# Kernel tuning notes

Hardware: AMD Instinct MI355X
Metric: run time of the kernel (lower is better)

The kernel has to match this reference:

```python
import jax, jax.numpy as jnp
import numpy as np

D_MODEL = 4096
N_Q_HEADS = 32
N_KV_HEADS = 8
HEAD_DIM = D_MODEL // N_Q_HEADS  # 128
N_REP = N_Q_HEADS // N_KV_HEADS  # 4
BATCH = 2
SEQ = 2048
ROPE_THETA = 10000.0


def setup_inputs() -> dict:
    key = jax.random.key(0)
    ks = jax.random.split(key, 5)
    scale = 0.02
    x = jax.random.normal(ks[0], (BATCH, SEQ, D_MODEL), dtype=jnp.float32)
    w_q = jax.random.normal(ks[1], (D_MODEL, N_Q_HEADS * HEAD_DIM), dtype=jnp.float32) * scale
    w_k = jax.random.normal(ks[2], (D_MODEL, N_KV_HEADS * HEAD_DIM), dtype=jnp.float32) * scale
    w_v = jax.random.normal(ks[3], (D_MODEL, N_KV_HEADS * HEAD_DIM), dtype=jnp.float32) * scale
    w_o = jax.random.normal(ks[4], (N_Q_HEADS * HEAD_DIM, D_MODEL), dtype=jnp.float32) * scale
    # precompute_theta_pos_freqs: freqs_cis = exp(1j * outer(t, inv_freq))
    inv_freq = 1.0 / (ROPE_THETA ** (jnp.arange(0, HEAD_DIM, 2)[: HEAD_DIM // 2] / HEAD_DIM))
    t = jnp.arange(SEQ, dtype=jnp.float32)
    freqs = jnp.outer(t, inv_freq)  # [S, HEAD_DIM//2]
    freqs_cos = jnp.cos(freqs).astype(jnp.float32)
    freqs_sin = jnp.sin(freqs).astype(jnp.float32)
    # additive causal mask [1,1,S,S]
    causal = jnp.tril(jnp.ones((SEQ, SEQ), dtype=bool))
    mask = jnp.where(causal, 0.0, -1e9).astype(jnp.float32)[None, None]
    return {"x": x, "w_q": w_q, "w_k": w_k, "w_v": w_v, "w_o": w_o,
            "freqs_cos": freqs_cos, "freqs_sin": freqs_sin, "mask": mask}


def _apply_rope(t, cos, sin):
    # t: [B,S,H,D]; cos/sin: [S,D//2]. Complex multiply in real arithmetic:
    # (a + bi) * (c + di) = (ac - bd) + (ad + bc)i
    B, S, H, D = t.shape
    tr = t.reshape(B, S, H, D // 2, 2)
    a, b = tr[..., 0], tr[..., 1]
    c = cos[None, :, None, :]
    s = sin[None, :, None, :]
    out = jnp.stack([a * c - b * s, a * s + b * c], axis=-1)
    return out.reshape(B, S, H, D)


def reference(x, w_q, w_k, w_v, w_o, freqs_cos, freqs_sin, mask):
    B, S, _ = x.shape
    xq = (x @ w_q).reshape(B, S, N_Q_HEADS, HEAD_DIM)
    xk = (x @ w_k).reshape(B, S, N_KV_HEADS, HEAD_DIM)
    xv = (x @ w_v).reshape(B, S, N_KV_HEADS, HEAD_DIM)
    xq = _apply_rope(xq, freqs_cos, freqs_sin)
    xk = _apply_rope(xk, freqs_cos, freqs_sin)
    # repeat_kv (tile+reshape == repeat along head axis)
    keys = jnp.repeat(xk, N_REP, axis=2)    # [B,S,Hq,D]
    values = jnp.repeat(xv, N_REP, axis=2)  # [B,S,Hq,D]
    xq = xq.transpose(0, 2, 1, 3)           # [B,Hq,S,D]
    keys = keys.transpose(0, 2, 1, 3)
    values = values.transpose(0, 2, 1, 3)
    scores = jnp.einsum("bhqd,bhkd->bhqk", xq, keys) / jnp.sqrt(
        jnp.asarray(HEAD_DIM, dtype=xq.dtype))
    scores = scores + mask
    probs = jax.nn.softmax(scores, axis=-1).astype(xq.dtype)
    out = jnp.einsum("bhqk,bhkd->bhqd", probs, values)
    out = out.transpose(0, 2, 1, 3).reshape(B, S, N_Q_HEADS * HEAD_DIM)
    return out @ w_o


if __name__ == "__main__":
    inp = setup_inputs()
    y = reference(**inp)
    print(y.shape, y.dtype)
```

## Files before the change

kernel.cpp:

```cpp
#include <hip/hip_runtime.h>
#include <stdint.h>
#include <stddef.h>


typedef __bf16 bf16x8 __attribute__((ext_vector_type(8)));
typedef float floatx4 __attribute__((ext_vector_type(4)));
typedef unsigned short ushort8v __attribute__((ext_vector_type(8)));
typedef unsigned short ushort4v __attribute__((ext_vector_type(4)));
typedef unsigned short ushort2v __attribute__((ext_vector_type(2)));

#define DEV static __device__ __forceinline__

DEV unsigned short f2bf(float f) {
  union { float f; unsigned u; } v; v.f = f;
  unsigned r = v.u + 0x7fffu + ((v.u >> 16) & 1u);
  return (unsigned short)(r >> 16);
}
DEV float bf2f(unsigned short b) {
  union { unsigned u; float f; } v; v.u = ((unsigned)b) << 16;
  return v.f;
}

DEV void gload_lds16(const void* g, void* lds) {
  __builtin_amdgcn_global_load_lds(
      (__attribute__((address_space(1))) void*)(g),
      (__attribute__((address_space(3))) void*)(lds), 16, 0, 0);
}

__global__ __launch_bounds__(256) void cvt_fp32_bf16(
    const float* __restrict__ in, unsigned short* __restrict__ out, int n4) {
  int i = blockIdx.x * 256 + threadIdx.x;
  if (i >= n4) return;
  float4 v = ((const float4*)in)[i];
  ushort4v w;
  w.x = f2bf(v.x); w.y = f2bf(v.y); w.z = f2bf(v.z); w.w = f2bf(v.w);
  *(ushort4v*)(out + (size_t)i * 4) = w;
}

__global__ __launch_bounds__(256) void transpose_cvt(
    const float* __restrict__ in, unsigned short* __restrict__ out, int K, int N) {
  __shared__ float tile[32][33];
  int k0 = blockIdx.x * 32, n0 = blockIdx.y * 32;
  int tx = threadIdx.x & 31, ty = threadIdx.x >> 5;
  for (int i = 0; i < 32; i += 8)
    tile[ty + i][tx] = in[(size_t)(k0 + ty + i) * N + n0 + tx];
  __syncthreads();
  for (int i = 0; i < 32; i += 8)
    out[(size_t)(n0 + ty + i) * K + k0 + tx] = f2bf(tile[tx][ty + i]);
}

template <int STORE_F32>
__global__ __launch_bounds__(256, 2) void gemm_bt(
    const unsigned short* __restrict__ A, const unsigned short* __restrict__ Bt,
    void* __restrict__ Cp, int M, int N, int K) {
  __shared__ __align__(16) unsigned short a_lds[4096];
  __shared__ __align__(16) unsigned short b_lds[4096];
  const int tid = threadIdx.x;
  const int wave = tid >> 6, lane = tid & 63;
  const int quad = lane >> 4, l16 = lane & 15;
  const int m0 = blockIdx.x * 128, n0 = blockIdx.y * 128;
  const int wm = (wave >> 1) * 64, wn = (wave & 1) * 64;

  const int srow = (lane >> 2);
  const int skq = (lane & 3) ^ ((lane >> 2) & 3);

  floatx4 acc[4][4] = {};

  for (int k0 = 0; k0 < K; k0 += 32) {
    __syncthreads();
    for (int s = 0; s < 2; ++s) {
      int t = wave * 2 + s;
      int row = t * 16 + srow;
      gload_lds16(A + (size_t)(m0 + row) * K + k0 + skq * 8, a_lds + t * 512);
      gload_lds16(Bt + (size_t)(n0 + row) * K + k0 + skq * 8, b_lds + t * 512);
    }
    __syncthreads();
    bf16x8 af[4], bfr[4];
    const int pos = (quad ^ (l16 & 3)) * 8;
    for (int i = 0; i < 4; ++i)
      af[i] = *(const bf16x8*)(a_lds + (wm + i * 16 + l16) * 32 + pos);
    for (int j = 0; j < 4; ++j)
      bfr[j] = *(const bf16x8*)(b_lds + (wn + j * 16 + l16) * 32 + pos);
    for (int i = 0; i < 4; ++i)
      for (int j = 0; j < 4; ++j)
        acc[i][j] =
            __builtin_amdgcn_mfma_f32_16x16x32_bf16(af[i], bfr[j], acc[i][j], 0, 0, 0);
  }

  for (int i = 0; i < 4; ++i)
    for (int j = 0; j < 4; ++j)
      for (int r = 0; r < 4; ++r) {
        int row = m0 + wm + i * 16 + quad * 4 + r;
        int col = n0 + wn + j * 16 + l16;
        float v = acc[i][j][r];
        if (STORE_F32)
          ((float*)Cp)[(size_t)row * N + col] = v;
        else
          ((unsigned short*)Cp)[(size_t)row * N + col] = f2bf(v);
      }
}

__global__ __launch_bounds__(256) void rope_q(
    const unsigned short* __restrict__ qkv, const float* __restrict__ fc,
    const float* __restrict__ fs, unsigned short* __restrict__ Qd) {
  int gid = blockIdx.x * 256 + threadIdx.x;
  int i = gid & 63;
  int h = (gid >> 6) & 31;
  int s = (gid >> 11) & 2047;
  int b = gid >> 22;
  int row = b * 2048 + s;
  ushort2v p = *(const ushort2v*)(qkv + (size_t)row * 6144 + h * 128 + 2 * i);
  float a = bf2f(p.x), bb = bf2f(p.y);
  float c = fc[s * 64 + i], sn = fs[s * 64 + i];
  ushort2v w;
  w.x = f2bf(a * c - bb * sn);
  w.y = f2bf(a * sn + bb * c);
  *(ushort2v*)(Qd + ((((size_t)b * 32 + h) * 2048 + s) * 128 + 2 * i)) = w;
}

__global__ __launch_bounds__(256) void rope_k(
    const unsigned short* __restrict__ qkv, const float* __restrict__ fc,
    const float* __restrict__ fs, unsigned short* __restrict__ Kd) {
  int gid = blockIdx.x * 256 + threadIdx.x;
  int i = gid & 63;
  int kvh = (gid >> 6) & 7;
  int s = (gid >> 9) & 2047;
  int b = gid >> 20;
  int row = b * 2048 + s;
  ushort2v p = *(const ushort2v*)(qkv + (size_t)row * 6144 + 4096 + kvh * 128 + 2 * i);
  float a = bf2f(p.x), bb = bf2f(p.y);
  float c = fc[s * 64 + i], sn = fs[s * 64 + i];
  ushort2v w;
  w.x = f2bf(a * c - bb * sn);
  w.y = f2bf(a * sn + bb * c);
  *(ushort2v*)(Kd + ((((size_t)b * 8 + kvh) * 2048 + s) * 128 + 2 * i)) = w;
}

__global__ __launch_bounds__(256) void vtrans(
    const unsigned short* __restrict__ qkv, unsigned short* __restrict__ Vt) {
  __shared__ unsigned short tile[32][33];
  int bk = blockIdx.z;
  int b = bk >> 3, kvh = bk & 7;
  int s0 = blockIdx.x * 32, d0 = blockIdx.y * 32;
  int tx = threadIdx.x & 31, ty = threadIdx.x >> 5;
  for (int i = 0; i < 32; i += 8)
    tile[ty + i][tx] =
        qkv[(size_t)(b * 2048 + s0 + ty + i) * 6144 + 5120 + kvh * 128 + d0 + tx];
  __syncthreads();
  for (int i = 0; i < 32; i += 8)
    Vt[((size_t)bk * 128 + d0 + ty + i) * 2048 + s0 + tx] = tile[tx][ty + i];
}

__global__ __launch_bounds__(512, 4) void attn_kernel(
    const unsigned short* __restrict__ Q,
    const unsigned short* __restrict__ Kd,
    const unsigned short* __restrict__ Vt,
    unsigned short* __restrict__ O) {
  __shared__ __align__(16) unsigned short k_lds[64][136];
  __shared__ __align__(16) unsigned short v_lds[128][72];
  __shared__ __align__(16) unsigned short p_lds[8][16][72];

  const int tid = threadIdx.x;
  const int wave = tid >> 6, lane = tid & 63;
  const int quad = lane >> 4, l16 = lane & 15;
  const int pr = blockIdx.x;
  const int h = blockIdx.y;
  const int b = blockIdx.z;
  const int kvh = h >> 2;
  const float scale = 0.08838834764831845f;

  const unsigned short* kbase = Kd + ((size_t)b * 8 + kvh) * 2048 * 128;
  const unsigned short* vbase = Vt + ((size_t)b * 8 + kvh) * 128 * 2048;

  const int kk = tid >> 4, kd = tid & 15;
  const int vd = tid >> 3, vs = tid & 7;

  for (int pass = 0; pass < 2; ++pass) {
    const int qt = pass == 0 ? pr : 15 - pr;
    const int q0 = qt * 128;

    const unsigned short* qrow =
        Q + (((size_t)b * 32 + h) * 2048 + q0 + wave * 16 + l16) * 128;
    bf16x8 qf[4];
    for (int t = 0; t < 4; ++t)
      qf[t] = *(const bf16x8*)(qrow + t * 32 + quad * 8);

    float m_i[4], l_i[4];
    for (int r = 0; r < 4; ++r) { m_i[r] = -3.0e38f; l_i[r] = 0.f; }
    floatx4 o_acc[8] = {};

    ushort8v krg[2], vrg[2];
    krg[0] = *(const ushort8v*)(kbase + (size_t)kk * 128 + kd * 8);
    krg[1] = *(const ushort8v*)(kbase + (size_t)(kk + 32) * 128 + kd * 8);
    vrg[0] = *(const ushort8v*)(vbase + (size_t)vd * 2048 + vs * 8);
    vrg[1] = *(const ushort8v*)(vbase + (size_t)(vd + 64) * 2048 + vs * 8);

    const int kb_last = q0 + 64;
    for (int kb = 0; kb <= kb_last; kb += 64) {
      __syncthreads();
      *(ushort8v*)&k_lds[kk][kd * 8] = krg[0];
      *(ushort8v*)&k_lds[kk + 32][kd * 8] = krg[1];
      *(ushort8v*)&v_lds[vd][vs * 8] = vrg[0];
      *(ushort8v*)&v_lds[vd + 64][vs * 8] = vrg[1];
      __syncthreads();
      if (kb < kb_last) {
        int nkb = kb + 64;
        krg[0] = *(const ushort8v*)(kbase + (size_t)(nkb + kk) * 128 + kd * 8);
        krg[1] = *(const ushort8v*)(kbase + (size_t)(nkb + kk + 32) * 128 + kd * 8);
        vrg[0] = *(const ushort8v*)(vbase + (size_t)vd * 2048 + nkb + vs * 8);
        vrg[1] = *(const ushort8v*)(vbase + (size_t)(vd + 64) * 2048 + nkb + vs * 8);
      }
      if (kb > q0 + wave * 16 + 15) continue;

      float sv[4][4];
      for (int kt = 0; kt < 4; ++kt) {
        floatx4 a = {0.f, 0.f, 0.f, 0.f};
        for (int t = 0; t < 4; ++t) {
          bf16x8 kf = *(const bf16x8*)&k_lds[kt * 16 + l16][t * 32 + quad * 8];
          a = __builtin_amdgcn_mfma_f32_16x16x32_bf16(qf[t], kf, a, 0, 0, 0);
        }
        for (int r = 0; r < 4; ++r) sv[kt][r] = a[r] * scale;
      }
      if (kb + 63 > q0 + wave * 16) {
        for (int kt = 0; kt < 4; ++kt) {
          int kcol = kb + kt * 16 + l16;
          for (int r = 0; r < 4; ++r) {
            int qg = q0 + wave * 16 + quad * 4 + r;
            if (kcol > qg) sv[kt][r] -= 1.0e9f;
          }
        }
      }
      float mx[4];
      for (int r = 0; r < 4; ++r) {
        float m = fmaxf(fmaxf(sv[0][r], sv[1][r]), fmaxf(sv[2][r], sv[3][r]));
        for (int off = 1; off < 16; off <<= 1)
          m = fmaxf(m, __shfl_xor(m, off));
        mx[r] = m;
      }
      bool grow = false;
      for (int r = 0; r < 4; ++r) grow |= (mx[r] > m_i[r] + 8.f);
      if (__any(grow)) {
        for (int r = 0; r < 4; ++r) {
          float mnew = fmaxf(m_i[r], mx[r]);
          float alpha = __expf(m_i[r] - mnew);
          m_i[r] = mnew;
          l_i[r] *= alpha;
          for (int nb = 0; nb < 8; ++nb) o_acc[nb][r] *= alpha;
        }
      }
      for (int r = 0; r < 4; ++r) {
        float sum = 0.f;
        for (int kt = 0; kt < 4; ++kt) {
          float p = __expf(sv[kt][r] - m_i[r]);
          sv[kt][r] = p;
          sum += p;
        }
        for (int off = 1; off < 16; off <<= 1)
          sum += __shfl_xor(sum, off);
        l_i[r] += sum;
      }
      for (int kt = 0; kt < 4; ++kt)
        for (int r = 0; r < 4; ++r)
          p_lds[wave][quad * 4 + r][kt * 16 + l16] = f2bf(sv[kt][r]);
      for (int tk = 0; tk < 2; ++tk) {
        bf16x8 pa = *(const bf16x8*)&p_lds[wave][l16][tk * 32 + quad * 8];
        for (int nb = 0; nb < 8; ++nb) {
          bf16x8 vb = *(const bf16x8*)&v_lds[nb * 16 + l16][tk * 32 + quad * 8];
          o_acc[nb] = __builtin_amdgcn_mfma_f32_16x16x32_bf16(pa, vb, o_acc[nb], 0, 0, 0);
        }
      }
    }

    for (int nb = 0; nb < 8; ++nb)
      for (int r = 0; r < 4; ++r) {
        int row = b * 2048 + q0 + wave * 16 + quad * 4 + r;
        int col = h * 128 + nb * 16 + l16;
        O[(size_t)row * 4096 + col] = f2bf(o_acc[nb][r] / l_i[r]);
      }
  }
}

extern "C" void kernel_launch(void* const* d_in, const int* in_sizes, int n_in,
                              void* d_out, int out_size, void* d_ws, size_t ws_size,
                              hipStream_t stream) {
  const float* x   = (const float*)d_in[0];
  const float* w_q = (const float*)d_in[1];
  const float* w_k = (const float*)d_in[2];
  const float* w_v = (const float*)d_in[3];
  const float* w_o = (const float*)d_in[4];
  const float* fc  = (const float*)d_in[5];
  const float* fs  = (const float*)d_in[6];
  (void)in_sizes; (void)n_in; (void)out_size; (void)ws_size;

  char* ws = (char*)d_ws;
  unsigned short* xb  = (unsigned short*)(ws);
  unsigned short* wT  = (unsigned short*)(ws + 33554432ull);
  unsigned short* qkv = (unsigned short*)(ws + 83886080ull);
  unsigned short* Kd  = (unsigned short*)(ws + 134217728ull);
  unsigned short* Vt  = (unsigned short*)(ws + 142606336ull);
  unsigned short* Qd  = xb;
  unsigned short* woT = wT;
  unsigned short* Ob  = qkv;

  cvt_fp32_bf16<<<16384, 256, 0, stream>>>(x, xb, 4194304);
  transpose_cvt<<<dim3(128, 128), 256, 0, stream>>>(w_q, wT, 4096, 4096);
  transpose_cvt<<<dim3(128, 32), 256, 0, stream>>>(w_k, wT + (size_t)4096 * 4096, 4096, 1024);
  transpose_cvt<<<dim3(128, 32), 256, 0, stream>>>(w_v, wT + (size_t)5120 * 4096, 4096, 1024);
  gemm_bt<0><<<dim3(32, 48), 256, 0, stream>>>(xb, wT, qkv, 4096, 6144, 4096);
  transpose_cvt<<<dim3(128, 128), 256, 0, stream>>>(w_o, woT, 4096, 4096);
  rope_q<<<32768, 256, 0, stream>>>(qkv, fc, fs, Qd);
  rope_k<<<8192, 256, 0, stream>>>(qkv, fc, fs, Kd);
  vtrans<<<dim3(64, 4, 16), 256, 0, stream>>>(qkv, Vt);
  attn_kernel<<<dim3(8, 32, 2), 512, 0, stream>>>(Qd, Kd, Vt, Ob);
  gemm_bt<1><<<dim3(32, 32), 256, 0, stream>>>(Ob, woT, d_out, 4096, 4096, 4096);
}
```

Measured before the change: 817.1 us.

## Replace GEMM with 256x256 tile, 8-wave, double-buffered ping-pong pipelined kernel

Replaces the 128x128 single-buffered GEMM with a 256x256-tile, 512-thread kernel. It uses K=64 double-buffered LDS with XOR swizzle, interleaves global-to-LDS staging with MFMA phases under barriers and s_setprio, and adds block-index swizzling for L2 locality. The aim is to raise arithmetic intensity and hide memory latency in the QKV and output projections. In exchange it uses 128KB of LDS and many more accumulator registers, and depends on hand-tuned vmcnt counts, so occupancy and correctness are sensitive.

New measurement: 794.3 us. 1.03x faster.

```diff
diff --git a/kernel.cpp b/kernel.cpp
--- a/kernel.cpp
+++ b/kernel.cpp
@@ -49,50 +49,132 @@
     out[(size_t)(n0 + ty + i) * K + k0 + tx] = f2bf(tile[tx][ty + i]);
 }
 
+#define LD8(LDS, D, ROW, Q)                                                  \
+  (*(const bf16x8*)((const char*)(LDS) + (D) * 32768 + (ROW) * 128 +         \
+                    (((Q) ^ ((ROW) & 7)) << 4)))
+
+#define STAGE(PANEL, LDS, KT, H)                                             \
+  {                                                                          \
+    _Pragma("unroll") for (int j_ = 0; j_ < 2; ++j_) {                       \
+      int t_ = wave * 2 + j_;                                                \
+      int row_ = (H) * 128 + t_ * 8 + srow;                                  \
+      gload_lds16(PANEL + (size_t)row_ * K + (size_t)(KT) * 64 + qsrc * 8,   \
+                  (char*)(LDS) + ((KT) & 1) * 32768 + (H) * 16384 +          \
+                      t_ * 1024);                                            \
+    }                                                                        \
+  }
+
+#define READ_A(D, MH)                                                        \
+  _Pragma("unroll") for (int mf_ = 0; mf_ < 4; ++mf_)                        \
+      _Pragma("unroll") for (int kk_ = 0; kk_ < 2; ++kk_)                    \
+          aR[mf_][kk_] =                                                     \
+      LD8(a_lds, D, wm + ((MH) * 4 + mf_) * 16 + l16, kk_ * 4 + quad);
+
+#define READ_B(D, NH, BREG)                                                  \
+  _Pragma("unroll") for (int nf_ = 0; nf_ < 2; ++nf_)                        \
+      _Pragma("unroll") for (int kk_ = 0; kk_ < 2; ++kk_)                    \
+          BREG[nf_][kk_] =                                                   \
+      LD8(b_lds, D, wn + ((NH) * 2 + nf_) * 16 + l16, kk_ * 4 + quad);
+
+#define MFMA_Q(MH, NH, BREG)                                                 \
+  _Pragma("unroll") for (int mf_ = 0; mf_ < 4; ++mf_)                        \
+      _Pragma("unroll") for (int nf_ = 0; nf_ < 2; ++nf_)                    \
+          _Pragma("unroll") for (int kk_ = 0; kk_ < 2; ++kk_)                \
+              acc[(MH) * 4 + mf_][(NH) * 2 + nf_] =                          \
+      __builtin_amdgcn_mfma_f32_16x16x32_bf16(                               \
+          aR[mf_][kk_], BREG[nf_][kk_],                                      \
+          acc[(MH) * 4 + mf_][(NH) * 2 + nf_], 0, 0, 0);
+
+#define PH_SYNC_BEGIN                                                        \
+  __builtin_amdgcn_s_barrier();                                              \
+  asm volatile("s_waitcnt lgkmcnt(0)" ::: "memory");                         \
+  __builtin_amdgcn_s_setprio(1);
+
+#define PH_SYNC_END                                                          \
+  __builtin_amdgcn_s_setprio(0);                                             \
+  __builtin_amdgcn_s_barrier();
+
 template <int STORE_F32>
-__global__ __launch_bounds__(256, 2) void gemm_bt(
+__global__ __launch_bounds__(512, 2) void gemm_bt8(
     const unsigned short* __restrict__ A, const unsigned short* __restrict__ Bt,
     void* __restrict__ Cp, int M, int N, int K) {
-  __shared__ __align__(16) unsigned short a_lds[4096];
-  __shared__ __align__(16) unsigned short b_lds[4096];
+  __shared__ __align__(16) unsigned short a_lds[32768];
+  __shared__ __align__(16) unsigned short b_lds[32768];
+
   const int tid = threadIdx.x;
   const int wave = tid >> 6, lane = tid & 63;
   const int quad = lane >> 4, l16 = lane & 15;
-  const int m0 = blockIdx.x * 128, n0 = blockIdx.y * 128;
-  const int wm = (wave >> 1) * 64, wn = (wave & 1) * 64;
-
-  const int srow = (lane >> 2);
-  const int skq = (lane & 3) ^ ((lane >> 2) & 3);
-
-  floatx4 acc[4][4] = {};
-
-  for (int k0 = 0; k0 < K; k0 += 32) {
-    __syncthreads();
-    for (int s = 0; s < 2; ++s) {
-      int t = wave * 2 + s;
-      int row = t * 16 + srow;
-      gload_lds16(A + (size_t)(m0 + row) * K + k0 + skq * 8, a_lds + t * 512);
-      gload_lds16(Bt + (size_t)(n0 + row) * K + k0 + skq * 8, b_lds + t * 512);
+  const int wm = (wave >> 2) * 128, wn = (wave & 3) * 64;
+
+  const int gx = gridDim.x, gy = gridDim.y;
+  int lid = blockIdx.y * gx + blockIdx.x;
+  int cpx = (gx * gy) >> 3;
+  int swz = (lid & 7) * cpx + (lid >> 3);
+  const int m0 = (swz / gy) * 256, n0 = (swz % gy) * 256;
+
+  const int qsrc = (lane & 7) ^ (lane >> 3);
+  const int srow = lane >> 3;
+  const unsigned short* Ab = A + (size_t)m0 * K;
+  const unsigned short* Bb = Bt + (size_t)n0 * K;
+
+  floatx4 acc[8][4] = {};
+  bf16x8 aR[4][2], bLo[2][2], bHi[2][2];
+
+  const int nt = K >> 6;
+  const int iters = nt >> 1;
+
+  STAGE(Ab, a_lds, 0, 0); STAGE(Ab, a_lds, 0, 1);
+  STAGE(Bb, b_lds, 0, 0); STAGE(Bb, b_lds, 0, 1);
+  STAGE(Bb, b_lds, 1, 0); STAGE(Bb, b_lds, 1, 1);
+  asm volatile("s_waitcnt vmcnt(0)" ::: "memory");
+  __builtin_amdgcn_s_barrier();
+
+  for (int i = 0; i < iters; ++i) {
+    const int t0 = 2 * i;
+    const bool has2 = (t0 + 2 < nt);
+    READ_A(0, 0); READ_B(0, 0, bLo);
+    STAGE(Ab, a_lds, t0 + 1, 0);
+    PH_SYNC_BEGIN; MFMA_Q(0, 0, bLo); PH_SYNC_END;
+    READ_B(0, 1, bHi);
+    STAGE(Ab, a_lds, t0 + 1, 1);
+    PH_SYNC_BEGIN; MFMA_Q(0, 1, bHi); PH_SYNC_END;
+    READ_A(0, 1);
+    if (has2) STAGE(Bb, b_lds, t0 + 2, 0);
+    PH_SYNC_BEGIN; MFMA_Q(1, 1, bHi); PH_SYNC_END;
+    if (has2) {
+      STAGE(Bb, b_lds, t0 + 2, 1);
+      asm volatile("s_waitcnt vmcnt(4)" ::: "memory");
+    } else {
+      asm volatile("s_waitcnt vmcnt(0)" ::: "memory");
     }
-    __syncthreads();
-    bf16x8 af[4], bfr[4];
-    const int pos = (quad ^ (l16 & 3)) * 8;
-    for (int i = 0; i < 4; ++i)
-      af[i] = *(const bf16x8*)(a_lds + (wm + i * 16 + l16) * 32 + pos);
-    for (int j = 0; j < 4; ++j)
-      bfr[j] = *(const bf16x8*)(b_lds + (wn + j * 16 + l16) * 32 + pos);
-    for (int i = 0; i < 4; ++i)
-      for (int j = 0; j < 4; ++j)
-        acc[i][j] =
-            __builtin_amdgcn_mfma_f32_16x16x32_bf16(af[i], bfr[j], acc[i][j], 0, 0, 0);
+    PH_SYNC_BEGIN; MFMA_Q(1, 0, bLo); PH_SYNC_END;
+    READ_A(1, 0); READ_B(1, 0, bLo);
+    if (has2) STAGE(Ab, a_lds, t0 + 2, 0);
+    PH_SYNC_BEGIN; MFMA_Q(0, 0, bLo); PH_SYNC_END;
+    READ_B(1, 1, bHi);
+    if (has2) STAGE(Ab, a_lds, t0 + 2, 1);
+    PH_SYNC_BEGIN; MFMA_Q(0, 1, bHi); PH_SYNC_END;
+    READ_A(1, 1);
+    if (has2) STAGE(Bb, b_lds, t0 + 3, 0);
+    PH_SYNC_BEGIN; MFMA_Q(1, 1, bHi); PH_SYNC_END;
+    if (has2) {
+      STAGE(Bb, b_lds, t0 + 3, 1);
+      asm volatile("s_waitcnt vmcnt(4)" ::: "memory");
+    } else {
+      asm volatile("s_waitcnt vmcnt(0)" ::: "memory");
+    }
+    PH_SYNC_BEGIN; MFMA_Q(1, 0, bLo); PH_SYNC_END;
   }
 
-  for (int i = 0; i < 4; ++i)
-    for (int j = 0; j < 4; ++j)
+#pragma unroll
+  for (int mf = 0; mf < 8; ++mf)
+#pragma unroll
+    for (int nf = 0; nf < 4; ++nf)
+#pragma unroll
       for (int r = 0; r < 4; ++r) {
-        int row = m0 + wm + i * 16 + quad * 4 + r;
-        int col = n0 + wn + j * 16 + l16;
-        float v = acc[i][j][r];
+        int row = m0 + wm + mf * 16 + quad * 4 + r;
+        int col = n0 + wn + nf * 16 + l16;
+        float v = acc[mf][nf][r];
         if (STORE_F32)
           ((float*)Cp)[(size_t)row * N + col] = v;
         else
@@ -306,11 +388,11 @@
   transpose_cvt<<<dim3(128, 128), 256, 0, stream>>>(w_q, wT, 4096, 4096);
   transpose_cvt<<<dim3(128, 32), 256, 0, stream>>>(w_k, wT + (size_t)4096 * 4096, 4096, 1024);
   transpose_cvt<<<dim3(128, 32), 256, 0, stream>>>(w_v, wT + (size_t)5120 * 4096, 4096, 1024);
-  gemm_bt<0><<<dim3(32, 48), 256, 0, stream>>>(xb, wT, qkv, 4096, 6144, 4096);
+  gemm_bt8<0><<<dim3(16, 24), 512, 0, stream>>>(xb, wT, qkv, 4096, 6144, 4096);
   transpose_cvt<<<dim3(128, 128), 256, 0, stream>>>(w_o, woT, 4096, 4096);
   rope_q<<<32768, 256, 0, stream>>>(qkv, fc, fs, Qd);
   rope_k<<<8192, 256, 0, stream>>>(qkv, fc, fs, Kd);
   vtrans<<<dim3(64, 4, 16), 256, 0, stream>>>(qkv, Vt);
   attn_kernel<<<dim3(8, 32, 2), 512, 0, stream>>>(Qd, Kd, Vt, Ob);
-  gemm_bt<1><<<dim3(32, 32), 256, 0, stream>>>(Ob, woT, d_out, 4096, 4096, 4096);
-}
+  gemm_bt8<1><<<dim3(16, 16), 512, 0, stream>>>(Ob, woT, d_out, 4096, 4096, 4096);
+}
```

## Rewrite GEMM with triple-buffered LDS pipeline, 256x128 tiles and XCD-aware mapping

Applied to the files above, without the earlier changes.

The bf16 GEMM used for the QKV and output projections is replaced with a 512-thread kernel using 256x128 block tiles. A three-stage LDS ring buffer prefetches two K-tiles ahead, with explicit vmcnt waits in place of two full syncthreads per iteration. Block indices are remapped so each XCD works on a contiguous region of the output, improving L2 reuse. MFMA sections are raised in priority with setprio. The deeper pipeline uses more LDS and relies on hand-counted waitcnts, which is fragile. The mapping assumes grid dimensions divisible by 2 and 4.

Measured after the change: 815.9 us. No clear change (-0.1%).

```diff
diff --git a/kernel.cpp b/kernel.cpp
--- a/kernel.cpp
+++ b/kernel.cpp
@@ -49,50 +49,108 @@
     out[(size_t)(n0 + ty + i) * K + k0 + tx] = f2bf(tile[tx][ty + i]);
 }
 
+#define GBAR __builtin_amdgcn_s_barrier()
+#define GSCHED0 __builtin_amdgcn_sched_barrier(0)
+#define GWAITL0                                                              \
+  asm volatile("s_waitcnt lgkmcnt(0)" ::: "memory");                         \
+  GSCHED0
+#define GVMC3 asm volatile("s_waitcnt vmcnt(3)" ::: "memory")
+#define GVMC0 asm volatile("s_waitcnt vmcnt(0)" ::: "memory")
+#define GPRIO1 __builtin_amdgcn_s_setprio(1)
+#define GPRIO0 __builtin_amdgcn_s_setprio(0)
+
+#define STAGE_A(KT, BUF)                                                     \
+  {                                                                          \
+    _Pragma("unroll") for (int h_ = 0; h_ < 2; ++h_) {                       \
+      int row_ = h_ * 128 + wave * 16 + srow;                                \
+      gload_lds16(Ab + (size_t)row_ * K + (KT) * 32 + qsrc * 8,              \
+                  (char*)a_lds + (BUF) * 16384 + h_ * 8192 + wave * 1024);   \
+    }                                                                        \
+  }
+#define STAGE_B(KT, BUF)                                                     \
+  {                                                                          \
+    int row_ = wave * 16 + srow;                                             \
+    gload_lds16(Bb + (size_t)row_ * K + (KT) * 32 + qsrc * 8,                \
+                (char*)b_lds + (BUF) * 8192 + wave * 1024);                  \
+  }
+
+#define RD_A(BUF)                                                            \
+  _Pragma("unroll") for (int mf_ = 0; mf_ < 4; ++mf_) {                      \
+    int r_ = wm + mf_ * 16 + l16;                                            \
+    aR[mf_] = *(const bf16x8*)((const char*)a_lds + (BUF) * 16384 +          \
+                               r_ * 64 + ((quad ^ (r_ & 3)) << 4));          \
+  }
+#define RD_B(BUF)                                                            \
+  _Pragma("unroll") for (int nf_ = 0; nf_ < 4; ++nf_) {                      \
+    int r_ = wn + nf_ * 16 + l16;                                            \
+    bR[nf_] = *(const bf16x8*)((const char*)b_lds + (BUF) * 8192 +           \
+                               r_ * 64 + ((quad ^ (r_ & 3)) << 4));          \
+  }
+
 template <int STORE_F32>
-__global__ __launch_bounds__(256, 2) void gemm_bt(
+__global__ __launch_bounds__(512, 4) void gemm_bt3(
     const unsigned short* __restrict__ A, const unsigned short* __restrict__ Bt,
     void* __restrict__ Cp, int M, int N, int K) {
-  __shared__ __align__(16) unsigned short a_lds[4096];
-  __shared__ __align__(16) unsigned short b_lds[4096];
+  __shared__ __align__(16) unsigned short a_lds[3 * 256 * 32];
+  __shared__ __align__(16) unsigned short b_lds[3 * 128 * 32];
+
   const int tid = threadIdx.x;
   const int wave = tid >> 6, lane = tid & 63;
   const int quad = lane >> 4, l16 = lane & 15;
-  const int m0 = blockIdx.x * 128, n0 = blockIdx.y * 128;
   const int wm = (wave >> 1) * 64, wn = (wave & 1) * 64;
 
-  const int srow = (lane >> 2);
-  const int skq = (lane & 3) ^ ((lane >> 2) & 3);
+  const int gx = gridDim.x, gy = gridDim.y;
+  int lid = blockIdx.y * gx + blockIdx.x;
+  int xcd = lid & 7, idx = lid >> 3;
+  int gm = gx >> 1, gn = gy >> 2;
+  int xm = xcd & 1, xn = xcd >> 1;
+  const int m0 = (xm * gm + idx % gm) * 256;
+  const int n0 = (xn * gn + idx / gm) * 128;
+
+  const int srow = lane >> 2;
+  const int qsrc = (lane & 3) ^ ((lane >> 2) & 3);
+  const unsigned short* Ab = A + (size_t)m0 * K;
+  const unsigned short* Bb = Bt + (size_t)n0 * K;
 
   floatx4 acc[4][4] = {};
-
-  for (int k0 = 0; k0 < K; k0 += 32) {
-    __syncthreads();
-    for (int s = 0; s < 2; ++s) {
-      int t = wave * 2 + s;
-      int row = t * 16 + srow;
-      gload_lds16(A + (size_t)(m0 + row) * K + k0 + skq * 8, a_lds + t * 512);
-      gload_lds16(Bt + (size_t)(n0 + row) * K + k0 + skq * 8, b_lds + t * 512);
-    }
-    __syncthreads();
-    bf16x8 af[4], bfr[4];
-    const int pos = (quad ^ (l16 & 3)) * 8;
-    for (int i = 0; i < 4; ++i)
-      af[i] = *(const bf16x8*)(a_lds + (wm + i * 16 + l16) * 32 + pos);
-    for (int j = 0; j < 4; ++j)
-      bfr[j] = *(const bf16x8*)(b_lds + (wn + j * 16 + l16) * 32 + pos);
-    for (int i = 0; i < 4; ++i)
-      for (int j = 0; j < 4; ++j)
-        acc[i][j] =
-            __builtin_amdgcn_mfma_f32_16x16x32_bf16(af[i], bfr[j], acc[i][j], 0, 0, 0);
-  }
-
-  for (int i = 0; i < 4; ++i)
-    for (int j = 0; j < 4; ++j)
+  bf16x8 aR[4], bR[4];
+
+  const int nt = K >> 5;
+
+  STAGE_A(0, 0); STAGE_B(0, 0);
+  STAGE_A(1, 1); STAGE_B(1, 1);
+  GVMC3;
+  GBAR;
+
+  int bc = 0, bn = 2;
+  for (int t = 0; t < nt; ++t) {
+    const bool hasS = (t + 2 < nt);
+    if (hasS) { STAGE_A(t + 2, bn); STAGE_B(t + 2, bn); }
+    RD_A(bc); RD_B(bc);
+    GWAITL0;
+    GPRIO1;
+#pragma unroll
+    for (int mf = 0; mf < 4; ++mf)
+#pragma unroll
+      for (int nf = 0; nf < 4; ++nf)
+        acc[mf][nf] = __builtin_amdgcn_mfma_f32_16x16x32_bf16(
+            aR[mf], bR[nf], acc[mf][nf], 0, 0, 0);
+    GPRIO0;
+    if (hasS) { GVMC3; } else { GVMC0; }
+    GBAR;
+    bc = bc == 2 ? 0 : bc + 1;
+    bn = bn == 2 ? 0 : bn + 1;
+  }
+
+#pragma unroll
+  for (int mf = 0; mf < 4; ++mf)
+#pragma unroll
+    for (int nf = 0; nf < 4; ++nf)
+#pragma unroll
       for (int r = 0; r < 4; ++r) {
-        int row = m0 + wm + i * 16 + quad * 4 + r;
-        int col = n0 + wn + j * 16 + l16;
-        float v = acc[i][j][r];
+        int row = m0 + wm + mf * 16 + quad * 4 + r;
+        int col = n0 + wn + nf * 16 + l16;
+        float v = acc[mf][nf][r];
         if (STORE_F32)
           ((float*)Cp)[(size_t)row * N + col] = v;
         else
@@ -306,11 +364,11 @@
   transpose_cvt<<<dim3(128, 128), 256, 0, stream>>>(w_q, wT, 4096, 4096);
   transpose_cvt<<<dim3(128, 32), 256, 0, stream>>>(w_k, wT + (size_t)4096 * 4096, 4096, 1024);
   transpose_cvt<<<dim3(128, 32), 256, 0, stream>>>(w_v, wT + (size_t)5120 * 4096, 4096, 1024);
-  gemm_bt<0><<<dim3(32, 48), 256, 0, stream>>>(xb, wT, qkv, 4096, 6144, 4096);
+  gemm_bt3<0><<<dim3(16, 48), 512, 0, stream>>>(xb, wT, qkv, 4096, 6144, 4096);
   transpose_cvt<<<dim3(128, 128), 256, 0, stream>>>(w_o, woT, 4096, 4096);
   rope_q<<<32768, 256, 0, stream>>>(qkv, fc, fs, Qd);
   rope_k<<<8192, 256, 0, stream>>>(qkv, fc, fs, Kd);
   vtrans<<<dim3(64, 4, 16), 256, 0, stream>>>(qkv, Vt);
   attn_kernel<<<dim3(8, 32, 2), 512, 0, stream>>>(Qd, Kd, Vt, Ob);
-  gemm_bt<1><<<dim3(32, 32), 256, 0, stream>>>(Ob, woT, d_out, 4096, 4096, 4096);
-}
+  gemm_bt3<1><<<dim3(16, 32), 512, 0, stream>>>(Ob, woT, d_out, 4096, 4096, 4096);
+}
```
